# Kernel optimization log

Hardware: AMD Instinct MI355X
Metric: run time of the kernel (lower is better)

Reference implementation:

```python
import jax, jax.numpy as jnp
import numpy as np

NUM_USERS = 4096
NUM_ITEMS = 4096
NUM_CLASSES = 5
INPUT_DIM = 64
H0 = 64   # hidden[0]
H1 = 32   # hidden[1]
BU = 2048
BV = 2048


def setup_inputs() -> dict:
    key = jax.random.key(0)
    ks = jax.random.split(key, 9)
    ridx = jax.random.randint(ks[0], (NUM_USERS, NUM_ITEMS), 0, NUM_CLASSES * 10)
    ratings = (jnp.arange(NUM_CLASSES)[:, None, None] == ridx[None]).astype(jnp.float32)
    u = jax.random.randint(ks[1], (BU,), 0, NUM_USERS)
    v = jax.random.randint(ks[2], (BV,), 0, NUM_ITEMS)
    u_emb = jax.random.normal(ks[3], (NUM_USERS, INPUT_DIM), jnp.float32) * 0.1
    v_emb = jax.random.normal(ks[4], (NUM_ITEMS, INPUT_DIM), jnp.float32) * 0.1
    gc_w = jax.random.normal(ks[5], (NUM_CLASSES, INPUT_DIM, H0), jnp.float32) / np.sqrt(INPUT_DIM)
    gc_b = jnp.zeros((NUM_CLASSES, H0), jnp.float32)
    dense_w = jax.random.normal(ks[6], (H0, H1), jnp.float32) / np.sqrt(H0)
    dense_b = jnp.zeros((H1,), jnp.float32)
    dec_w = jax.random.normal(ks[7], (NUM_CLASSES, H1, H1), jnp.float32) / np.sqrt(H1)
    return dict(u=u, v=v, ratings=ratings, u_emb=u_emb, v_emb=v_emb,
                gc_w=gc_w, gc_b=gc_b, dense_w=dense_w, dense_b=dense_b, dec_w=dec_w)


def reference(u, v, ratings, u_emb, v_emb, gc_w, gc_b, dense_w, dense_b, dec_w):
    bu = u.shape[0]
    # m = index_select(index_select(ratings, 1, u), 2, v)  -> [C, bu, bv]
    m = ratings[:, u][:, :, v]
    ue = u_emb[u]                      # [bu, D]
    ve = v_emb[v]                      # [bv, D]
    # Degree normalization exactly as in the torch code:
    # du = |sum over dim1 then dim0| -> per-item counts [bv]; di -> per-user counts [bu]
    du = jnp.abs(jnp.sum(m, axis=(0, 1)))
    di = jnp.abs(jnp.sum(m, axis=(0, 2)))
    c = jnp.concatenate([du, di])      # [bv + bu] (requires bu == bv, as in original)
    c = jnp.where(c > 0, 1.0 / c, 0.0)
    x = jnp.concatenate([ue, ve], axis=0)              # [bu+bv, D]
    # Per-class graph convolution, summed over rating classes.
    support = jnp.einsum('nd,cdh->cnh', x, gc_w)       # [C, N, H0]
    su, sv = support[:, :bu], support[:, bu:]
    agg_u = jnp.einsum('cuv,cvh->cuh', m, sv)          # users aggregate items
    agg_v = jnp.einsum('cuv,cuh->cvh', m, su)          # items aggregate users
    agg = jnp.concatenate([agg_u, agg_v], axis=1)      # [C, N, H0]
    z = jnp.sum(c[None, :, None] * agg + gc_b[:, None, :], axis=0)
    z = jax.nn.relu(z)
    hidden = jax.nn.sigmoid(z @ dense_w + dense_b)     # [N, H1]
    hu, hv = hidden[:bu], hidden[bu:]
    # Bilinear decoder: per-class logits u^T W_c v  -> [C, bu, bv]
    logits = jnp.einsum('ud,cde,ve->cuv', hu, dec_w, hv)
    probs = jax.nn.softmax(logits, axis=0)
    classes = jnp.arange(NUM_CLASSES, dtype=hidden.dtype)
    m_hat = jnp.einsum('c,cuv->uv', classes, probs)    # expected rating
    observed = jnp.sum(m, axis=0)                      # [bu, bv] in {0,1}
    n_obs = jnp.maximum(jnp.sum(observed), 1.0)
    logp = jax.nn.log_softmax(logits, axis=0)
    loss = -jnp.sum(m * logp) / n_obs
    pred = jnp.argmax(logits, axis=0)
    true = jnp.argmax(m, axis=0)
    accuracy = jnp.sum((pred == true) * observed) / n_obs
    return m_hat, loss, accuracy
```

## Files before the change

### kernel.cpp

```cpp
#include <hip/hip_runtime.h>
#include <hip/hip_bf16.h>
#include <cstdint>

#define RST 16777216
typedef unsigned short u16;
typedef unsigned char u8;
typedef unsigned int u32;
typedef unsigned long long u64;
typedef __attribute__((ext_vector_type(8))) short short8v;
typedef __attribute__((ext_vector_type(4))) float f32x4;

__device__ __forceinline__ u16 f2bf(float x){
  unsigned int b = __float_as_uint(x);
  unsigned int r = (b + 0x7FFFu + ((b >> 16) & 1u)) >> 16;
  return (u16)r;
}
__device__ __forceinline__ float bf2f(u16 h){
  return __uint_as_float(((unsigned int)h) << 16);
}
__device__ __forceinline__ void split8(const float* fa, short8v& hi, short8v& lo){
#pragma unroll
  for (int e = 0; e < 8; e++){
    u16 h = f2bf(fa[e]);
    hi[e] = (short)h;
    lo[e] = (short)f2bf(fa[e] - bf2f(h));
  }
}
__device__ __forceinline__ int cnt_not5(u32 w){
  int c = 0;
  c += ((w & 255u) != 5u); c += (((w >> 8) & 255u) != 5u);
  c += (((w >> 16) & 255u) != 5u); c += ((w >> 24) != 5u);
  return c;
}

__global__ __launch_bounds__(256) void k_labels(const int* __restrict__ u, const int* __restrict__ v,
                                                const float* __restrict__ ratings, u8* __restrict__ L,
                                                int* __restrict__ di){
  __shared__ float row[4096];
  __shared__ int wsum[4];
  int i = blockIdx.x;
  int tid = threadIdx.x;
  int lane = tid & 63, wid = tid >> 6;
  int U = u[i];
  int j0 = tid * 8;
  int vj[8];
#pragma unroll
  for (int k = 0; k < 8; k++) vj[k] = v[j0 + k];
  int lab[8];
#pragma unroll
  for (int k = 0; k < 8; k++) lab[k] = 5;
  const float* rbase = ratings + (size_t)U * 4096;
  for (int c = 0; c < 5; c++){
    const float4* src = (const float4*)(rbase + (size_t)c * RST);
#pragma unroll
    for (int k = 0; k < 4; k++) ((float4*)row)[tid + k*256] = src[tid + k*256];
    __syncthreads();
#pragma unroll
    for (int k = 0; k < 8; k++) if (row[vj[k]] > 0.5f) lab[k] = c;
    __syncthreads();
  }
  unsigned int lo = 0, hi = 0;
  int cnt = 0;
#pragma unroll
  for (int k = 0; k < 4; k++){
    lo |= ((unsigned)lab[k]) << (8*k); hi |= ((unsigned)lab[k+4]) << (8*k);
    cnt += (lab[k] != 5); cnt += (lab[k+4] != 5);
  }
  *(uint2*)(L + (size_t)i * 2048 + j0) = make_uint2(lo, hi);
#pragma unroll
  for (int o = 32; o > 0; o >>= 1) cnt += __shfl_down(cnt, o);
  if (lane == 0) wsum[wid] = cnt;
  __syncthreads();
  if (tid == 0) di[i] = wsum[0] + wsum[1] + wsum[2] + wsum[3];
}

__global__ __launch_bounds__(256) void k_trsup(const u8* __restrict__ L, u8* __restrict__ LT,
    const int* __restrict__ u, const int* __restrict__ v,
    const float* __restrict__ u_emb, const float* __restrict__ v_emb, const float* __restrict__ gc_w,
    u32* __restrict__ SPF){
  __shared__ union { u8 tile[64][64]; u32 pack[4096]; } sm;
  int tid = threadIdx.x;
  if (blockIdx.x < 1024){
    int jb = blockIdx.x & 31, ib = blockIdx.x >> 5;
    int i0 = ib * 64, j0 = jb * 64;
    int r = tid >> 2, cq = tid & 3;
    uint4 d = *(const uint4*)(L + (size_t)(i0 + r) * 2048 + j0 + cq * 16);
    *(uint4*)&sm.tile[r][cq * 16] = d;
    __syncthreads();
    u8 ob[16];
#pragma unroll
    for (int k = 0; k < 16; k++) ob[k] = sm.tile[cq * 16 + k][r];
    *(uint4*)(LT + (size_t)(j0 + r) * 2048 + i0 + cq * 16) = *(uint4*)ob;
  } else {
    int b = blockIdx.x - 1024;
    int c = b >> 6, nblk = b & 63;
    int lane = tid & 63, wv = tid >> 6;
    int m = lane & 15, q = lane >> 4;
    int n0 = nblk * 64;
    bool uside = (n0 < 2048);
    const int* nidx = uside ? u : v;
    const float* emb = uside ? u_emb : v_emb;
    int nbase = uside ? n0 : (n0 - 2048);
    int h0 = wv * 16;
    short8v bh[2], bl[2];
#pragma unroll
    for (int ch = 0; ch < 2; ch++){
      const float* wp = gc_w + c * 4096 + (ch * 32 + q * 8) * 64 + h0 + m;
      float fb[8];
#pragma unroll
      for (int e = 0; e < 8; e++) fb[e] = wp[e * 64];
      split8(fb, bh[ch], bl[ch]);
    }
#pragma unroll
    for (int rt = 0; rt < 4; rt++){
      const float* xr = emb + (size_t)nidx[nbase + rt * 16 + m] * 64;
      f32x4 acc = {0.f, 0.f, 0.f, 0.f};
#pragma unroll
      for (int ch = 0; ch < 2; ch++){
        float fa[8];
        *(float4*)&fa[0] = *(const float4*)(xr + ch * 32 + q * 8);
        *(float4*)&fa[4] = *(const float4*)(xr + ch * 32 + q * 8 + 4);
        short8v ah, al;
        split8(fa, ah, al);
        acc = __builtin_amdgcn_mfma_f32_16x16x32_bf16(ah, bh[ch], acc, 0, 0, 0);
        acc = __builtin_amdgcn_mfma_f32_16x16x32_bf16(ah, bl[ch], acc, 0, 0, 0);
        acc = __builtin_amdgcn_mfma_f32_16x16x32_bf16(al, bh[ch], acc, 0, 0, 0);
      }
#pragma unroll
      for (int reg = 0; reg < 4; reg++){
        float val = acc[reg];
        u16 vh = f2bf(val);
        u16 vl = f2bf(val - bf2f(vh));
        int n = n0 + rt * 16 + q * 4 + reg;
        int jc_l = (n >> 5) & 1;
        int kk = n & 31;
        int lanep = m + ((kk >> 3) << 4);
        int ep = kk & 7;
        sm.pack[((jc_l * 4 + wv) * 64 + lanep) * 8 + ep] = (((u32)vh) << 16) | (u32)vl;
      }
    }
    __syncthreads();
    int jc0 = n0 >> 5;
    u32* dst = SPF + ((size_t)(c * 128 + jc0) * 4) * 512;
#pragma unroll
    for (int p = 0; p < 4; p++){
      int t = p * 1024 + tid * 4;
      *(uint4*)&dst[t] = *(const uint4*)&sm.pack[t];
    }
  }
}

__global__ __launch_bounds__(512) void k_agg(const u8* __restrict__ L, const u8* __restrict__ LT,
    const u32* __restrict__ SPF, float* __restrict__ aggp){
  __shared__ u8 As[128][272];
  int tid = threadIdx.x;
  int lane = tid & 63, wv = tid >> 6;
  int half = wv >> 2, ht = wv & 3;
  int m = lane & 15, q = lane >> 4;
  int bid = blockIdx.x;
  int kc = bid & 7;
  int rb = bid >> 3;
  int r0 = rb * 128;
  bool uside = (r0 < 2048);
  const u8* Ab = uside ? (L + (size_t)r0 * 2048) : (LT + (size_t)(r0 - 2048) * 2048);
  int jcb = (uside ? 64 : 0) + kc * 8;
#pragma unroll
  for (int p = 0; p < 4; p++){
    int idx = p * 512 + tid;
    int row = idx >> 4, ci = idx & 15;
    *(uint4*)&As[row][ci * 16] = *(const uint4*)(Ab + (size_t)row * 2048 + kc * 256 + ci * 16);
  }
  __syncthreads();
  f32x4 acc[4];
#pragma unroll
  for (int it = 0; it < 4; it++) acc[it] = (f32x4){0.f, 0.f, 0.f, 0.f};
  for (int ks = 0; ks < 8; ks++){
    short8v bh[5], bl[5];
#pragma unroll
    for (int c = 0; c < 5; c++){
      const uint4* bp = (const uint4*)(SPF + ((size_t)((c * 128 + jcb + ks) * 4 + ht) * 64 + lane) * 8);
      uint4 wA = bp[0], wB = bp[1];
      u32 wws[8] = {wA.x, wA.y, wA.z, wA.w, wB.x, wB.y, wB.z, wB.w};
#pragma unroll
      for (int e = 0; e < 8; e++){
        bh[c][e] = (short)(wws[e] >> 16);
        bl[c][e] = (short)(wws[e] & 0xffffu);
      }
    }
#pragma unroll
    for (int it = 0; it < 4; it++){
      u64 a8 = *(const u64*)&As[half * 64 + it * 16 + m][ks * 32 + q * 8];
      int b[8];
#pragma unroll
      for (int e = 0; e < 8; e++) b[e] = (int)((a8 >> (8 * e)) & 255u);
#pragma unroll
      for (int c = 0; c < 5; c++){
        short8v am;
#pragma unroll
        for (int e = 0; e < 8; e++) am[e] = (short)((b[e] == c) ? 0x3F80 : 0);
        acc[it] = __builtin_amdgcn_mfma_f32_16x16x32_bf16(am, bh[c], acc[it], 0, 0, 0);
        acc[it] = __builtin_amdgcn_mfma_f32_16x16x32_bf16(am, bl[c], acc[it], 0, 0, 0);
      }
    }
  }
  float* op = aggp + (size_t)kc * 262144;
  int h0 = ht * 16;
#pragma unroll
  for (int it = 0; it < 4; it++){
#pragma unroll
    for (int reg = 0; reg < 4; reg++)
      op[(size_t)(r0 + half * 64 + it * 16 + q * 4 + reg) * 64 + h0 + m] = acc[it][reg];
  }
}

__global__ __launch_bounds__(256) void k_hidden(const float* __restrict__ aggp, const u8* __restrict__ LT,
    const int* __restrict__ di,
    const float* __restrict__ gc_b, const float* __restrict__ dense_w, const float* __restrict__ dense_b,
    float* __restrict__ hidden){
  int wid = threadIdx.x >> 6, lane = threadIdx.x & 63;
  int r = blockIdx.x * 4 + wid;
  float a = 0.f;
#pragma unroll
  for (int kc = 0; kc < 8; kc++) a += aggp[(size_t)kc * 262144 + (size_t)r * 64 + lane];
  int cnt;
  if (r < 2048){
    const uint4* rp = (const uint4*)(LT + (size_t)r * 2048);
    uint4 w1 = rp[lane * 2], w2 = rp[lane * 2 + 1];
    int c2 = cnt_not5(w1.x) + cnt_not5(w1.y) + cnt_not5(w1.z) + cnt_not5(w1.w)
           + cnt_not5(w2.x) + cnt_not5(w2.y) + cnt_not5(w2.z) + cnt_not5(w2.w);
#pragma unroll
    for (int o = 32; o > 0; o >>= 1) c2 += __shfl_down(c2, o);
    cnt = __shfl(c2, 0);
  } else {
    cnt = di[r - 2048];
  }
  float inv = (cnt > 0) ? (1.0f / (float)cnt) : 0.0f;
  float bsum = 0.f;
#pragma unroll
  for (int c = 0; c < 5; c++) bsum += gc_b[c * 64 + lane];
  float z = fmaxf(a * inv + bsum, 0.f);
  __shared__ float zb[4][64];
  zb[wid][lane] = z;
  __syncthreads();
  if (lane < 32){
    float s = dense_b[lane];
#pragma unroll
    for (int h = 0; h < 64; h++) s += zb[wid][h] * dense_w[h * 32 + lane];
    hidden[(size_t)r * 32 + lane] = 1.0f / (1.0f + __expf(-s));
  }
}

#define EPI(l, lab, outp) do{ \
  float mx = fmaxf(fmaxf(fmaxf(l[0], l[1]), fmaxf(l[2], l[3])), l[4]); \
  float e0 = __expf(l[0]-mx), e1 = __expf(l[1]-mx), e2 = __expf(l[2]-mx), e3 = __expf(l[3]-mx), e4 = __expf(l[4]-mx); \
  float ssum = e0 + e1 + e2 + e3 + e4; \
  *(outp) = (e1 + 2.f*e2 + 3.f*e3 + 4.f*e4) / ssum; \
  if ((lab) < 5){ \
    int pred = 0; float bm = l[0]; \
    if (l[1] > bm){ bm = l[1]; pred = 1; } \
    if (l[2] > bm){ bm = l[2]; pred = 2; } \
    if (l[3] > bm){ bm = l[3]; pred = 3; } \
    if (l[4] > bm){ bm = l[4]; pred = 4; } \
    float ll = (lab)==0 ? l[0] : ((lab)==1 ? l[1] : ((lab)==2 ? l[2] : ((lab)==3 ? l[3] : l[4]))); \
    lsum += __logf(ssum) + mx - ll; \
    acnt += (pred == (lab)); \
  } \
}while(0)

__global__ __launch_bounds__(256) void k_logits(const float* __restrict__ hidden, const float* __restrict__ dec_w,
    const u8* __restrict__ L, float* __restrict__ mhat, float* __restrict__ lpart, int* __restrict__ apart){
  __shared__ float hu_s[512];
  __shared__ float tsf[5 * 16 * 36];
  int tid = threadIdx.x;
  int lane = tid & 63, w = tid >> 6;
  int i0 = blockIdx.y * 16;
  if (tid < 128) ((float4*)hu_s)[tid] = ((const float4*)(hidden + (size_t)i0 * 32))[tid];
  __syncthreads();
  for (int idx = tid; idx < 2560; idx += 256){
    int c = idx >> 9; int rem = idx & 511; int ii = rem >> 5; int e = rem & 31;
    const float* wc = dec_w + (size_t)c * 1024 + e;
    const float* hr = hu_s + ii * 32;
    float s = 0.f;
#pragma unroll
    for (int d = 0; d < 32; d++) s += hr[d] * wc[d * 32];
    tsf[(c * 16 + ii) * 36 + e] = s;
  }
  __syncthreads();
  int m = lane & 15, q = lane >> 4;
  short8v a_hi[5], a_lo[5];
#pragma unroll
  for (int c = 0; c < 5; c++){
    const float* p = &tsf[(c * 16 + m) * 36 + q * 8];
    float fa[8];
    *(float4*)&fa[0] = *(const float4*)p;
    *(float4*)&fa[4] = *(const float4*)(p + 4);
    split8(fa, a_hi[c], a_lo[c]);
  }
  const float* hv = hidden + 2048 * 32;
  float lsum = 0.f; int acnt = 0;
  int jw0 = blockIdx.x * 256 + w * 64;
#pragma unroll
  for (int jj = 0; jj < 4; jj++){
    int j0 = jw0 + jj * 16;
    const float* pb = hv + (size_t)(j0 + m) * 32 + q * 8;
    float fb[8];
    *(float4*)&fb[0] = *(const float4*)pb;
    *(float4*)&fb[4] = *(const float4*)(pb + 4);
    short8v b_hi, b_lo;
    split8(fb, b_hi, b_lo);
    f32x4 acc[5];
    f32x4 z4 = {0.f, 0.f, 0.f, 0.f};
#pragma unroll
    for (int c = 0; c < 5; c++){
      f32x4 a = __builtin_amdgcn_mfma_f32_16x16x32_bf16(a_hi[c], b_hi, z4, 0, 0, 0);
      a = __builtin_amdgcn_mfma_f32_16x16x32_bf16(a_hi[c], b_lo, a, 0, 0, 0);
      a = __builtin_amdgcn_mfma_f32_16x16x32_bf16(a_lo[c], b_hi, a, 0, 0, 0);
      acc[c] = a;
    }
    int jcol = j0 + m;
#pragma unroll
    for (int r = 0; r < 4; r++){
      int irow = i0 + q * 4 + r;
      float l5[5] = {acc[0][r], acc[1][r], acc[2][r], acc[3][r], acc[4][r]};
      int lab = L[(size_t)irow * 2048 + jcol];
      EPI(l5, lab, mhat + (size_t)irow * 2048 + jcol);
    }
  }
#pragma unroll
  for (int o = 32; o > 0; o >>= 1){ lsum += __shfl_down(lsum, o); acnt += __shfl_down(acnt, o); }
  __shared__ float wl[4]; __shared__ int wa[4];
  if (lane == 0){ wl[w] = lsum; wa[w] = acnt; }
  __syncthreads();
  if (tid == 0){
    int pb = blockIdx.y * 8 + blockIdx.x;
    lpart[pb] = wl[0] + wl[1] + wl[2] + wl[3];
    apart[pb] = wa[0] + wa[1] + wa[2] + wa[3];
  }
}

__global__ __launch_bounds__(256) void k_final(const float* __restrict__ lpart, const int* __restrict__ apart,
                                               const int* __restrict__ di, float* __restrict__ out){
  __shared__ float lred[256];
  __shared__ int ared[256], nred[256];
  int tid = threadIdx.x;
  float ls = 0.f; int as = 0;
#pragma unroll
  for (int k = 0; k < 4; k++){ ls += lpart[tid + k * 256]; as += apart[tid + k * 256]; }
  int ns = 0;
#pragma unroll
  for (int k = 0; k < 8; k++) ns += di[tid + k * 256];
  lred[tid] = ls; ared[tid] = as; nred[tid] = ns;
  __syncthreads();
  for (int s = 128; s > 0; s >>= 1){
    if (tid < s){ lred[tid] += lred[tid + s]; ared[tid] += ared[tid + s]; nred[tid] += nred[tid + s]; }
    __syncthreads();
  }
  if (tid == 0){
    float n = fmaxf((float)nred[0], 1.0f);
    out[0] = lred[0] / n;
    out[1] = ((float)ared[0]) / n;
  }
}

extern "C" void kernel_launch(void* const* d_in, const int* in_sizes, int n_in,
                              void* d_out, int out_size, void* d_ws, size_t ws_size,
                              hipStream_t stream){
  const int*   u       = (const int*)d_in[0];
  const int*   v       = (const int*)d_in[1];
  const float* ratings = (const float*)d_in[2];
  const float* u_emb   = (const float*)d_in[3];
  const float* v_emb   = (const float*)d_in[4];
  const float* gc_w    = (const float*)d_in[5];
  const float* gc_b    = (const float*)d_in[6];
  const float* dense_w = (const float*)d_in[7];
  const float* dense_b = (const float*)d_in[8];
  const float* dec_w   = (const float*)d_in[9];
  float* out = (float*)d_out;
  char* ws = (char*)d_ws;

  u8*    L       = (u8*)(ws + 0);
  u8*    LT      = (u8*)(ws + 4194304);
  u32*   SPF     = (u32*)(ws + 8388608);
  float* aggp    = (float*)(ws + 13631488);
  float* hidden  = (float*)(ws + 22020096);
  int*   di      = (int*)(ws + 22544384);
  float* lpart   = (float*)(ws + 22552576);
  int*   apart   = (int*)(ws + 22556672);

  k_labels <<<2048, 256, 0, stream>>>(u, v, ratings, L, di);
  k_trsup  <<<1344, 256, 0, stream>>>(L, LT, u, v, u_emb, v_emb, gc_w, SPF);
  k_agg    <<<256, 512, 0, stream>>>(L, LT, SPF, aggp);
  k_hidden <<<1024, 256, 0, stream>>>(aggp, LT, di, gc_b, dense_w, dense_b, hidden);
  k_logits <<<dim3(8, 128), 256, 0, stream>>>(hidden, dec_w, L, out, lpart, apart);
  k_final  <<<1, 256, 0, stream>>>(lpart, apart, di, out + 4194304);
}
```

Baseline: 94.62 us.

## Split support into hi/lo bf16 planes and remap agg warps to row tiles

The interleaved hi/lo u32 support buffer is replaced by two separate bf16 planes, so k_agg loads short8 vectors directly and no longer needs shift/mask unpacking. In k_agg each wave now owns one 16-row tile and all four 16-wide hidden tiles, so the one-hot A fragments are built once per k-step and reused across ht. Before, the B fragments were reused across four row tiles. Block ordering also changes so that consecutive blocks walk row blocks within the same k-chunk, which may improve L2 reuse of the support data. In exchange, each wave loads 20 B fragments per k-step from global memory instead of 5, which raises global and L2 traffic.

Measured after the change: 152.1 us. 1.61x slower.

```diff
diff --git a/kernel.cpp b/kernel.cpp
--- a/kernel.cpp
+++ b/kernel.cpp
@@ -77,8 +77,8 @@
 __global__ __launch_bounds__(256) void k_trsup(const u8* __restrict__ L, u8* __restrict__ LT,
     const int* __restrict__ u, const int* __restrict__ v,
     const float* __restrict__ u_emb, const float* __restrict__ v_emb, const float* __restrict__ gc_w,
-    u32* __restrict__ SPF){
-  __shared__ union { u8 tile[64][64]; u32 pack[4096]; } sm;
+    u16* __restrict__ SPFh, u16* __restrict__ SPFl){
+  __shared__ union { u8 tile[64][64]; struct { u16 h[4096]; u16 l[4096]; } pk; } sm;
   int tid = threadIdx.x;
   if (blockIdx.x < 1024){
     int jb = blockIdx.x & 31, ib = blockIdx.x >> 5;
@@ -136,30 +136,33 @@
         int kk = n & 31;
         int lanep = m + ((kk >> 3) << 4);
         int ep = kk & 7;
-        sm.pack[((jc_l * 4 + wv) * 64 + lanep) * 8 + ep] = (((u32)vh) << 16) | (u32)vl;
+        int pidx = ((jc_l * 4 + wv) * 64 + lanep) * 8 + ep;
+        sm.pk.h[pidx] = vh;
+        sm.pk.l[pidx] = vl;
       }
     }
     __syncthreads();
     int jc0 = n0 >> 5;
-    u32* dst = SPF + ((size_t)(c * 128 + jc0) * 4) * 512;
-#pragma unroll
-    for (int p = 0; p < 4; p++){
-      int t = p * 1024 + tid * 4;
-      *(uint4*)&dst[t] = *(const uint4*)&sm.pack[t];
+    u16* dsth = SPFh + (size_t)(c * 128 + jc0) * 2048;
+    u16* dstl = SPFl + (size_t)(c * 128 + jc0) * 2048;
+#pragma unroll
+    for (int p = 0; p < 2; p++){
+      int t = p * 256 + tid;
+      ((uint4*)dsth)[t] = ((const uint4*)sm.pk.h)[t];
+      ((uint4*)dstl)[t] = ((const uint4*)sm.pk.l)[t];
     }
   }
 }
 
 __global__ __launch_bounds__(512) void k_agg(const u8* __restrict__ L, const u8* __restrict__ LT,
-    const u32* __restrict__ SPF, float* __restrict__ aggp){
+    const u16* __restrict__ SPFh, const u16* __restrict__ SPFl, float* __restrict__ aggp){
   __shared__ u8 As[128][272];
   int tid = threadIdx.x;
   int lane = tid & 63, wv = tid >> 6;
-  int half = wv >> 2, ht = wv & 3;
   int m = lane & 15, q = lane >> 4;
   int bid = blockIdx.x;
-  int kc = bid & 7;
-  int rb = bid >> 3;
+  int rb = bid & 31;
+  int kc = bid >> 5;
   int r0 = rb * 128;
   bool uside = (r0 < 2048);
   const u8* Ab = uside ? (L + (size_t)r0 * 2048) : (LT + (size_t)(r0 - 2048) * 2048);
@@ -173,43 +176,38 @@
   __syncthreads();
   f32x4 acc[4];
 #pragma unroll
-  for (int it = 0; it < 4; it++) acc[it] = (f32x4){0.f, 0.f, 0.f, 0.f};
+  for (int ht = 0; ht < 4; ht++) acc[ht] = (f32x4){0.f, 0.f, 0.f, 0.f};
   for (int ks = 0; ks < 8; ks++){
-    short8v bh[5], bl[5];
+    u64 a8 = *(const u64*)&As[wv * 16 + m][ks * 32 + q * 8];
+    int b[8];
+#pragma unroll
+    for (int e = 0; e < 8; e++) b[e] = (int)((a8 >> (8 * e)) & 255u);
+    short8v am[5];
 #pragma unroll
     for (int c = 0; c < 5; c++){
-      const uint4* bp = (const uint4*)(SPF + ((size_t)((c * 128 + jcb + ks) * 4 + ht) * 64 + lane) * 8);
-      uint4 wA = bp[0], wB = bp[1];
-      u32 wws[8] = {wA.x, wA.y, wA.z, wA.w, wB.x, wB.y, wB.z, wB.w};
-#pragma unroll
-      for (int e = 0; e < 8; e++){
-        bh[c][e] = (short)(wws[e] >> 16);
-        bl[c][e] = (short)(wws[e] & 0xffffu);
+#pragma unroll
+      for (int e = 0; e < 8; e++) am[c][e] = (short)((b[e] == c) ? 0x3F80 : 0);
+    }
+    const u16* baseh = SPFh + (size_t)(jcb + ks) * 2048 * 4 / 4;
+#pragma unroll
+    for (int ht = 0; ht < 4; ht++){
+#pragma unroll
+      for (int c = 0; c < 5; c++){
+        size_t fo = ((size_t)((c * 128 + jcb + ks) * 4 + ht) * 64 + lane) * 8;
+        short8v bhv = *(const short8v*)(SPFh + fo);
+        short8v blv = *(const short8v*)(SPFl + fo);
+        acc[ht] = __builtin_amdgcn_mfma_f32_16x16x32_bf16(am[c], bhv, acc[ht], 0, 0, 0);
+        acc[ht] = __builtin_amdgcn_mfma_f32_16x16x32_bf16(am[c], blv, acc[ht], 0, 0, 0);
       }
     }
-#pragma unroll
-    for (int it = 0; it < 4; it++){
-      u64 a8 = *(const u64*)&As[half * 64 + it * 16 + m][ks * 32 + q * 8];
-      int b[8];
-#pragma unroll
-      for (int e = 0; e < 8; e++) b[e] = (int)((a8 >> (8 * e)) & 255u);
-#pragma unroll
-      for (int c = 0; c < 5; c++){
-        short8v am;
-#pragma unroll
-        for (int e = 0; e < 8; e++) am[e] = (short)((b[e] == c) ? 0x3F80 : 0);
-        acc[it] = __builtin_amdgcn_mfma_f32_16x16x32_bf16(am, bh[c], acc[it], 0, 0, 0);
-        acc[it] = __builtin_amdgcn_mfma_f32_16x16x32_bf16(am, bl[c], acc[it], 0, 0, 0);
-      }
-    }
-  }
+  }
+  (void)sizeof(0);
   float* op = aggp + (size_t)kc * 262144;
-  int h0 = ht * 16;
-#pragma unroll
-  for (int it = 0; it < 4; it++){
+#pragma unroll
+  for (int ht = 0; ht < 4; ht++){
 #pragma unroll
     for (int reg = 0; reg < 4; reg++)
-      op[(size_t)(r0 + half * 64 + it * 16 + q * 4 + reg) * 64 + h0 + m] = acc[it][reg];
+      op[(size_t)(r0 + wv * 16 + q * 4 + reg) * 64 + ht * 16 + m] = acc[ht][reg];
   }
 }
 
@@ -380,7 +378,8 @@
 
   u8*    L       = (u8*)(ws + 0);
   u8*    LT      = (u8*)(ws + 4194304);
-  u32*   SPF     = (u32*)(ws + 8388608);
+  u16*   SPFh    = (u16*)(ws + 8388608);
+  u16*   SPFl    = (u16*)(ws + 11010048);
   float* aggp    = (float*)(ws + 13631488);
   float* hidden  = (float*)(ws + 22020096);
   int*   di      = (int*)(ws + 22544384);
@@ -388,8 +387,8 @@
   int*   apart   = (int*)(ws + 22556672);
 
   k_labels <<<2048, 256, 0, stream>>>(u, v, ratings, L, di);
-  k_trsup  <<<1344, 256, 0, stream>>>(L, LT, u, v, u_emb, v_emb, gc_w, SPF);
-  k_agg    <<<256, 512, 0, stream>>>(L, LT, SPF, aggp);
+  k_trsup  <<<1344, 256, 0, stream>>>(L, LT, u, v, u_emb, v_emb, gc_w, SPFh, SPFl);
+  k_agg    <<<256, 512, 0, stream>>>(L, LT, SPFh, SPFl, aggp);
   k_hidden <<<1024, 256, 0, stream>>>(aggp, LT, di, gc_b, dense_w, dense_b, hidden);
   k_logits <<<dim3(8, 128), 256, 0, stream>>>(hidden, dec_w, L, out, lpart, apart);
   k_final  <<<1, 256, 0, stream>>>(lpart, apart, di, out + 4194304);
```
